# Kernel tuning notes

Hardware: AMD Instinct MI355X
Metric: run time of the kernel (lower is better)

## Reference

```python
import jax, jax.numpy as jnp
import numpy as np

EMA_DECAY = 0.99
LAPLACE_EPS = 1e-7
PERPLEXITY_EPS = 1e-10
COMMIT_COEF = 0.25


def setup_inputs() -> dict:
    key = jax.random.key(0)
    k1, k2, k3, k4 = jax.random.split(key, 4)
    B, C, T, H, W = 8, 256, 4, 32, 32
    n_codes = 2048
    z = jax.random.normal(k1, (B, C, T, H, W), dtype=jnp.float32)
    embeddings = jax.random.normal(k2, (n_codes, C), dtype=jnp.float32)
    N = jnp.ones((n_codes,), dtype=jnp.float32)  # state after _init_embeddings
    z_avg = jax.random.normal(k3, (n_codes, C), dtype=jnp.float32)
    k_rand = jax.random.normal(k4, (n_codes, C), dtype=jnp.float32)  # stand-in for randperm restart rows
    return {"z": z, "embeddings": embeddings, "N": N, "z_avg": z_avg, "k_rand": k_rand}


def reference(z, embeddings, N, z_avg, k_rand):
    b, c, t, h, w = z.shape
    n_codes = embeddings.shape[0]
    # rearrange 'b c t h w -> (b t h w) c'
    flat = jnp.transpose(z, (0, 2, 3, 4, 1)).reshape(-1, c)  # [Ntok, c]
    d2 = ((flat * flat).sum(axis=1, keepdims=True)
          - 2.0 * (flat @ embeddings.T)
          + (embeddings * embeddings).sum(axis=1)[None, :])  # [Ntok, n_codes]
    idx = jnp.argmin(d2, axis=1)  # [Ntok] int
    quant_flat = embeddings[idx]  # gather, [Ntok, c]
    # back to [b, c, t, h, w] (the double-rearrange in the torch code is a net permute back)
    quant = jnp.transpose(quant_flat.reshape(b, t, h, w, c), (0, 4, 1, 2, 3))
    commitment_loss = COMMIT_COEF * jnp.mean((z - jax.lax.stop_gradient(quant)) ** 2)
    embeddings_st = jax.lax.stop_gradient(quant - z) + z  # straight-through
    # EMA codebook update (one-hot scatter expressed as segment_sum)
    ones = jnp.ones(flat.shape[0], dtype=flat.dtype)
    counts = jax.ops.segment_sum(ones, idx, num_segments=n_codes)          # n_total
    encode_sum = jax.ops.segment_sum(flat, idx, num_segments=n_codes)      # [n_codes, c]
    new_N = N * EMA_DECAY + (1.0 - EMA_DECAY) * counts
    new_z_avg = z_avg * EMA_DECAY + (1.0 - EMA_DECAY) * encode_sum
    n = new_N.sum()
    weights = (new_N + LAPLACE_EPS) / (n + n_codes * LAPLACE_EPS) * n
    new_embeddings = new_z_avg / weights[:, None]
    usage = (new_N[:, None] >= 1.0).astype(flat.dtype)
    new_embeddings = new_embeddings * usage + k_rand * (1.0 - usage)
    # perplexity
    avg_probs = counts / flat.shape[0]
    perplexity = jnp.exp(-jnp.sum(avg_probs * jnp.log(avg_probs + PERPLEXITY_EPS)))
    encodings = idx.reshape(b, t, h, w)
    return embeddings_st, encodings, commitment_loss, perplexity, new_embeddings, new_N, new_z_avg
```

## Files before the change

### kernel.cpp

```cpp
#include <hip/hip_runtime.h>
#include <math.h>

#define NCODES 2048
#define CDIM   256
#define SPAT   4096
#define NTOK   32768
#define XSTR   260
#define EPI_TOK 32

#define ETILE    32
#define HALFCODE 1024
#define NTILES   (HALFCODE / ETILE)

typedef _Float16 half8  __attribute__((ext_vector_type(8)));
typedef float    f32x4  __attribute__((ext_vector_type(4)));

#define WS_ENORM  0
#define WS_COUNTS 2048
#define WS_LOSS   4096
#define WS_N      4097
#define WS_ESUM   4100
#define WS_IDX    528388
#define WS_OFF    561156
#define WS_CUR    563204
#define WS_SORT   565252
#define WS_SCODE  598020
#define WS_CAND   630788
#define WS_E16    761860
#define WS_XH     1024004

#define O_QUANT 0
#define O_ENC   8388608
#define O_LOSS  8421376
#define O_PERP  8421377
#define O_EMB   8421378
#define O_NN    8945666
#define O_ZAVG  8947714

__device__ inline void gl_lds16(const void* g, void* l) {
    __builtin_amdgcn_global_load_lds(
        (const __attribute__((address_space(1))) void*)g,
        (__attribute__((address_space(3))) void*)l, 16, 0, 0);
}

__device__ inline unsigned umn(unsigned a, unsigned b) { return a < b ? a : b; }
__device__ inline unsigned umx(unsigned a, unsigned b) { return a > b ? a : b; }
__device__ inline unsigned shflx16(unsigned v, int off) {
    return (unsigned)__shfl_xor((int)v, off, 16);
}

__global__ void k_ecvt(const float* __restrict__ emb, float* __restrict__ ws) {
    const int tid  = threadIdx.x;
    const int code = (blockIdx.x << 3) + (tid >> 5);
    const int cg   = tid & 31;
    const float* src = emb + (size_t)code * CDIM + (cg << 3);
    const float4 f0 = *(const float4*)src;
    const float4 f1 = *(const float4*)(src + 4);
    half8 h = { (_Float16)f0.x, (_Float16)f0.y, (_Float16)f0.z, (_Float16)f0.w,
                (_Float16)f1.x, (_Float16)f1.y, (_Float16)f1.z, (_Float16)f1.w };
    char* dst = (char*)(ws + WS_E16) + (size_t)code * 512 + ((cg ^ (code & 7)) << 4);
    *(half8*)dst = h;
    float s = f0.x * f0.x + f0.y * f0.y + f0.z * f0.z + f0.w * f0.w
            + f1.x * f1.x + f1.y * f1.y + f1.z * f1.z + f1.w * f1.w;
#pragma unroll
    for (int off = 16; off; off >>= 1) s += __shfl_down(s, off, 32);
    if (cg == 0) ws[WS_ENORM + code] = s;
}

__global__ __launch_bounds__(256, 3) void k_main(
    const float* __restrict__ z, float* __restrict__ ws)
{
    __shared__ half8 Es8[2][ETILE][32];

    const int tid = threadIdx.x;
    const int raw = blockIdx.x;
    const int xcd = raw & 7, sub = raw >> 3;
    const int tb  = xcd * 32 + (sub >> 1);
    const int ch  = sub & 1;
    const int b   = tb >> 5;
    const int s0  = (tb & 31) * 128;
    const float* zb = z + (size_t)b * CDIM * SPAT + s0;
    const char* e16g = (const char*)(ws + WS_E16) + (size_t)ch * HALFCODE * 512;

    const int l  = tid & 63, w = tid >> 6;
    const int lr = l & 15, lg = l >> 4;

    {
        char* dst = (char*)&Es8[0][0][0];
#pragma unroll
        for (int q = 0; q < 4; ++q) {
            const int off = ((q << 2) + w) << 10;
            gl_lds16(e16g + off + (l << 4), dst + off);
        }
    }

    half8 a[2][8];
#pragma unroll
    for (int as = 0; as < 2; ++as)
#pragma unroll
    for (int ks = 0; ks < 8; ++ks) {
        float v[8];
#pragma unroll
        for (int e = 0; e < 8; ++e)
            v[e] = zb[(size_t)(ks * 32 + lg * 8 + e) * SPAT + (w * 32 + as * 16 + lr)];
        half8 h = { (_Float16)v[0], (_Float16)v[1], (_Float16)v[2], (_Float16)v[3],
                    (_Float16)v[4], (_Float16)v[5], (_Float16)v[6], (_Float16)v[7] };
        a[as][ks] = h;
    }

    if (ch == 0) {
        _Float16* xh = (_Float16*)(ws + WS_XH);
#pragma unroll
        for (int as = 0; as < 2; ++as) {
            _Float16* xr = xh + (size_t)(b * SPAT + s0 + w * 32 + as * 16 + lr) * CDIM;
#pragma unroll
            for (int ks = 0; ks < 8; ++ks)
                *(half8*)(xr + ks * 32 + lg * 8) = a[as][ks];
        }
    }

    unsigned kb0[2][4], kb1[2][4];
#pragma unroll
    for (int as = 0; as < 2; ++as)
#pragma unroll
    for (int r = 0; r < 4; ++r) { kb0[as][r] = 0xFFFFFFFFu; kb1[as][r] = 0xFFFFFFFFu; }

    __syncthreads();

    int p = 0;
    for (int tile = 0; tile < NTILES; ++tile) {
        if (tile < NTILES - 1) {
            const char* src = e16g + (size_t)(tile + 1) * (ETILE * 512);
            char* dst = (char*)&Es8[p ^ 1][0][0];
#pragma unroll
            for (int q = 0; q < 4; ++q) {
                const int off = ((q << 2) + w) << 10;
                gl_lds16(src + off + (l << 4), dst + off);
            }
        }

        const float en0 = ws[WS_ENORM + ch * HALFCODE + tile * ETILE + lr];
        const float en1 = ws[WS_ENORM + ch * HALFCODE + tile * ETILE + 16 + lr];

        f32x4 acc[2][2];
#pragma unroll
        for (int as = 0; as < 2; ++as)
#pragma unroll
        for (int j = 0; j < 2; ++j) acc[as][j] = (f32x4)0.0f;

        half8 bf0[2], bf1[2];
#pragma unroll
        for (int j = 0; j < 2; ++j) {
            const int row = j * 16 + lr;
            bf0[j] = Es8[p][row][lg ^ (row & 7)];
        }
#pragma unroll
        for (int ks = 0; ks < 8; ++ks) {
            if (ks < 7) {
#pragma unroll
                for (int j = 0; j < 2; ++j) {
                    const int row = j * 16 + lr;
                    if (ks & 1) bf0[j] = Es8[p][row][((ks + 1) * 4 + lg) ^ (row & 7)];
                    else        bf1[j] = Es8[p][row][((ks + 1) * 4 + lg) ^ (row & 7)];
                }
            }
            __builtin_amdgcn_s_setprio(1);
#pragma unroll
            for (int as = 0; as < 2; ++as)
#pragma unroll
            for (int j = 0; j < 2; ++j)
                acc[as][j] = __builtin_amdgcn_mfma_f32_16x16x32_f16(
                    a[as][ks], (ks & 1) ? bf1[j] : bf0[j], acc[as][j], 0, 0, 0);
            __builtin_amdgcn_s_setprio(0);
        }

        const float enb0 = en0 + 4096.0f;
        const float enb1 = en1 + 4096.0f;
        const unsigned code0 = (unsigned)(ch * HALFCODE + tile * ETILE + lr);
        const unsigned code1 = code0 + 16u;
#pragma unroll
        for (int as = 0; as < 2; ++as)
#pragma unroll
        for (int r = 0; r < 4; ++r) {
            {
                const float d = fmaf(acc[as][0][r], -2.0f, enb0);
                const unsigned key = (__float_as_uint(d) & 0xFFFFF800u) | code0;
                const unsigned hi = umx(kb0[as][r], key);
                kb0[as][r] = umn(kb0[as][r], key);
                kb1[as][r] = umn(kb1[as][r], hi);
            }
            {
                const float d = fmaf(acc[as][1][r], -2.0f, enb1);
                const unsigned key = (__float_as_uint(d) & 0xFFFFF800u) | code1;
                const unsigned hi = umx(kb0[as][r], key);
                kb0[as][r] = umn(kb0[as][r], key);
                kb1[as][r] = umn(kb1[as][r], hi);
            }
        }

        __syncthreads();
        p ^= 1;
    }

#pragma unroll
    for (int as = 0; as < 2; ++as)
#pragma unroll
    for (int r = 0; r < 4; ++r) {
        unsigned k0 = kb0[as][r], k1 = kb1[as][r];
        unsigned k2 = 0xFFFFFFFFu, k3 = 0xFFFFFFFFu;
#pragma unroll
        for (int off = 8; off; off >>= 1) {
            const unsigned o0 = shflx16(k0, off);
            const unsigned o1 = shflx16(k1, off);
            const unsigned o2 = shflx16(k2, off);
            const unsigned o3 = shflx16(k3, off);
            const unsigned m0 = umn(k0, o3), m1 = umn(k1, o2);
            const unsigned m2 = umn(k2, o1), m3 = umn(k3, o0);
            const unsigned t0 = umn(m0, m2), t2 = umx(m0, m2);
            const unsigned t1 = umn(m1, m3), t3 = umx(m1, m3);
            k0 = umn(t0, t1); k1 = umx(t0, t1);
            k2 = umn(t2, t3); k3 = umx(t2, t3);
        }
        if (lr == 0) {
            const int tokg = b * SPAT + s0 + w * 32 + as * 16 + lg * 4 + r;
            ushort4 c4;
            c4.x = (unsigned short)(k0 & 2047u);
            c4.y = (unsigned short)(k1 & 2047u);
            c4.z = (unsigned short)(k2 & 2047u);
            c4.w = (unsigned short)(k3 & 2047u);
            *(ushort4*)((unsigned short*)((int*)ws + WS_CAND) + (size_t)tokg * 8 + ch * 4) = c4;
        }
    }
}

__global__ __launch_bounds__(256, 4) void k_epi(
    const float* __restrict__ z, const float* __restrict__ emb,
    float* __restrict__ ws, float* __restrict__ out)
{
    __shared__ float Xs[EPI_TOK * XSTR];
    __shared__ int   idxs[EPI_TOK];
    __shared__ float lloss[EPI_TOK];

    const int tid = threadIdx.x, blk = blockIdx.x;
    const int b   = blk >> 7;
    const int s0  = (blk & 127) * EPI_TOK;
    const float* zb = z + (size_t)b * CDIM * SPAT + s0;

    {
        const int s  = tid & 31;
        const int c0 = tid >> 5;
#pragma unroll 4
        for (int c = c0; c < CDIM; c += 8)
            Xs[s * XSTR + c] = zb[(size_t)c * SPAT + s];
    }
    __syncthreads();

    {
        const int t = tid >> 3, h = tid & 7;
        const unsigned short* cp =
            (const unsigned short*)((int*)ws + WS_CAND) + ((size_t)blk * EPI_TOK + t) * 8;
        const int mycand = cp[h];
        const float en_h = ws[WS_ENORM + mycand];

        int cand[8];
        {
            const ushort4 ca = *(const ushort4*)cp;
            const ushort4 cb = *(const ushort4*)(cp + 4);
            cand[0] = ca.x; cand[1] = ca.y; cand[2] = ca.z; cand[3] = ca.w;
            cand[4] = cb.x; cand[5] = cb.y; cand[6] = cb.z; cand[7] = cb.w;
        }

        float4 xq[8];
#pragma unroll
        for (int q = 0; q < 8; ++q)
            xq[q] = *(const float4*)&Xs[t * XSTR + q * 32 + h * 4];

        float xn = 0.0f;
#pragma unroll
        for (int q = 0; q < 8; ++q)
            xn += xq[q].x * xq[q].x + xq[q].y * xq[q].y
                + xq[q].z * xq[q].z + xq[q].w * xq[q].w;
        xn += __shfl_xor(xn, 1, 8);
        xn += __shfl_xor(xn, 2, 8);
        xn += __shfl_xor(xn, 4, 8);

        float p8[8];
#pragma unroll
        for (int k = 0; k < 8; ++k) {
            const float* er = emb + (size_t)cand[k] * CDIM + h * 4;
            float dp = 0.0f;
#pragma unroll
            for (int q = 0; q < 8; ++q) {
                const float4 e4 = *(const float4*)(er + q * 32);
                dp += xq[q].x * e4.x + xq[q].y * e4.y + xq[q].z * e4.z + xq[q].w * e4.w;
            }
            p8[k] = dp;
        }

        float np4[4];
#pragma unroll
        for (int k2 = 0; k2 < 4; ++k2) {
            const float own = (h & 1) ? p8[2 * k2 + 1] : p8[2 * k2];
            const float snd = (h & 1) ? p8[2 * k2]     : p8[2 * k2 + 1];
            np4[k2] = own + __shfl_xor(snd, 1, 8);
        }
        float nq2[2];
#pragma unroll
        for (int k3 = 0; k3 < 2; ++k3) {
            const float own = ((h >> 1) & 1) ? np4[2 * k3 + 1] : np4[2 * k3];
            const float snd = ((h >> 1) & 1) ? np4[2 * k3]     : np4[2 * k3 + 1];
            nq2[k3] = own + __shfl_xor(snd, 2, 8);
        }
        const float own = ((h >> 2) & 1) ? nq2[1] : nq2[0];
        const float snd = ((h >> 2) & 1) ? nq2[0] : nq2[1];
        const float dot = own + __shfl_xor(snd, 4, 8);

        float bd = en_h - 2.0f * dot;
        int   bi = mycand;
#pragma unroll
        for (int off = 4; off; off >>= 1) {
            const float od = __shfl_xor(bd, off, 8);
            const int   oi = __shfl_xor(bi, off, 8);
            if (od < bd || (od == bd && oi < bi)) { bd = od; bi = oi; }
        }
        if (h == 0) {
            idxs[t]  = bi;
            lloss[t] = xn + bd;
            out[O_ENC + blk * EPI_TOK + t] = (float)bi;
            ((int*)ws)[WS_IDX + blk * EPI_TOK + t] = bi;
            atomicAdd(ws + WS_COUNTS + bi, 1.0f);
        }
    }
    __syncthreads();

    {
        const int t = tid >> 3, h = tid & 7;
        const float* ewin = emb + (size_t)idxs[t] * CDIM + h * 4;
#pragma unroll
        for (int q = 0; q < 8; ++q)
            *(float4*)&Xs[t * XSTR + q * 32 + h * 4] = *(const float4*)(ewin + q * 32);
    }
    __syncthreads();

    {
        const int s  = tid & 31;
        const int c0 = tid >> 5;
        float* qcol = out + O_QUANT + (size_t)b * CDIM * SPAT + s0 + s;
#pragma unroll 4
        for (int c = c0; c < CDIM; c += 8)
            qcol[(size_t)c * SPAT] = Xs[s * XSTR + c];
    }
    if (tid == 0) {
        float ls = 0.0f;
#pragma unroll
        for (int t = 0; t < EPI_TOK; ++t) ls += lloss[t];
        atomicAdd(ws + WS_LOSS, ls);
    }
}

__global__ void k_finalize(const float* __restrict__ Nin, float* __restrict__ ws,
                           float* __restrict__ out) {
    __shared__ float r1[4], r2[4];
    __shared__ int   wsum[4];
    const int tid  = threadIdx.x;
    const int base = tid * 8;

    float cnt[8];
    {
        const float4 c0 = *(const float4*)(ws + WS_COUNTS + base);
        const float4 c1 = *(const float4*)(ws + WS_COUNTS + base + 4);
        cnt[0] = c0.x; cnt[1] = c0.y; cnt[2] = c0.z; cnt[3] = c0.w;
        cnt[4] = c1.x; cnt[5] = c1.y; cnt[6] = c1.z; cnt[7] = c1.w;
    }

    float nsum = 0.0f, H = 0.0f;
    int   tsum = 0;
#pragma unroll
    for (int j = 0; j < 8; ++j) {
        const float cf = cnt[j];
        const float nn = Nin[base + j] * 0.99f + 0.01f * cf;
        out[O_NN + base + j] = nn;
        nsum += nn;
        const float p = cf * (1.0f / 32768.0f);
        H += p * logf(p + 1e-10f);
        tsum += (int)cf;
    }

    int inc = tsum;
#pragma unroll
    for (int off = 1; off < 64; off <<= 1) {
        const int v = __shfl_up(inc, off, 64);
        if ((tid & 63) >= off) inc += v;
    }
    const int wv = tid >> 6, ln = tid & 63;
    if (ln == 63) wsum[wv] = inc;

#pragma unroll
    for (int off = 32; off; off >>= 1) {
        nsum += __shfl_down(nsum, off);
        H    += __shfl_down(H, off);
    }
    if (ln == 0) { r1[wv] = nsum; r2[wv] = H; }
    __syncthreads();

    int wbase = 0;
    for (int q = 0; q < wv; ++q) wbase += wsum[q];
    int run = wbase + inc - tsum;
    int* offp = (int*)ws + WS_OFF;
    int* curp = (int*)ws + WS_CUR;
#pragma unroll
    for (int j = 0; j < 8; ++j) {
        offp[base + j] = run;
        curp[base + j] = run;
        run += (int)cnt[j];
    }

    if (tid == 0) {
        const float nt = r1[0] + r1[1] + r1[2] + r1[3];
        const float Ht = r2[0] + r2[1] + r2[2] + r2[3];
        ws[WS_N] = nt;
        out[O_PERP] = expf(-Ht);
        out[O_LOSS] = 0.25f * ws[WS_LOSS] * (1.0f / 8388608.0f);
    }
}

__global__ void k_scatter(float* __restrict__ ws) {
    const int t    = blockIdx.x * 256 + threadIdx.x;
    const int code = ((const int*)ws)[WS_IDX + t];
    const int slot = atomicAdd((int*)ws + WS_CUR + code, 1);
    ((int*)ws)[WS_SORT  + slot] = t;
    ((int*)ws)[WS_SCODE + slot] = code;
}

__global__ __launch_bounds__(256) void k_gather(float* __restrict__ ws) {
    __shared__ int stok[64], scod[64];
    const int g = blockIdx.x, tid = threadIdx.x, c = tid;
    if (tid < 64) {
        stok[tid] = ((const int*)ws)[WS_SORT  + g * 64 + tid];
        scod[tid] = ((const int*)ws)[WS_SCODE + g * 64 + tid];
    }
    __syncthreads();

    const _Float16* xh = (const _Float16*)(ws + WS_XH);
    float* esum = ws + WS_ESUM;

    float acc = 0.0f;
    for (int k0 = 0; k0 < 64; k0 += 8) {
        float v[8];
#pragma unroll
        for (int j = 0; j < 8; ++j)
            v[j] = (float)xh[(size_t)stok[k0 + j] * CDIM + c];
#pragma unroll
        for (int j = 0; j < 8; ++j) {
            const int k = k0 + j;
            acc += v[j];
            if (k == 63 || scod[k] != scod[k + 1]) {
                atomicAdd(&esum[(size_t)scod[k] * CDIM + c], acc);
                acc = 0.0f;
            }
        }
    }
}

__global__ __launch_bounds__(256) void k_update(
    const float* __restrict__ zavg, const float* __restrict__ krand,
    const float* __restrict__ ws, float* __restrict__ out)
{
    const int i = blockIdx.x, c = threadIdx.x;
    const float nn  = out[O_NN + i];
    const float n   = ws[WS_N];
    const float wgt = (nn + 1e-7f) / (n + NCODES * 1e-7f) * n;
    const size_t o  = (size_t)i * CDIM + c;
    const float ez  = 0.99f * zavg[o] + 0.01f * ws[WS_ESUM + o];
    out[O_ZAVG + o] = ez;
    out[O_EMB + o]  = (nn >= 1.0f) ? (ez / wgt) : krand[o];
}

extern "C" void kernel_launch(void* const* d_in, const int* in_sizes, int n_in,
                              void* d_out, int out_size, void* d_ws, size_t ws_size,
                              hipStream_t stream) {
    const float* z     = (const float*)d_in[0];
    const float* emb   = (const float*)d_in[1];
    const float* Nin   = (const float*)d_in[2];
    const float* zavg  = (const float*)d_in[3];
    const float* krand = (const float*)d_in[4];
    float* out = (float*)d_out;
    float* ws  = (float*)d_ws;

    hipMemsetAsync(ws + WS_COUNTS, 0,
                   (size_t)(2048 + 4 + NCODES * CDIM) * sizeof(float), stream);

    k_ecvt    <<<NCODES / 8,  256, 0, stream>>>(emb, ws);
    k_main    <<<512,         256, 0, stream>>>(z, ws);
    k_epi     <<<1024,        256, 0, stream>>>(z, emb, ws, out);
    k_finalize<<<1,           256, 0, stream>>>(Nin, ws, out);
    k_scatter <<<NTOK / 256,  256, 0, stream>>>(ws);
    k_gather  <<<NTOK / 64,   256, 0, stream>>>(ws);
    k_update  <<<NCODES,      256, 0, stream>>>(zavg, krand, ws, out);
}
```

Measured before the change: 136.4 us.

## Triple-buffer codebook tiles in LDS with two-deep prefetch and partial waitcnt

Switches the codebook tile staging in the distance kernel from double to triple buffering, issuing async global-to-LDS loads two tiles ahead. Barriers wait only for the older batch of loads (vmcnt(4)) instead of draining all loads before every tile. The aim is to hide more global load latency behind the MFMA work. The cost is 50% more LDS per block, which may limit occupancy, and the hand-written vmcnt counts must stay correct, since the ws enorm loads also count as vector memory operations.

```diff
diff --git a/kernel.cpp b/kernel.cpp
--- a/kernel.cpp
+++ b/kernel.cpp
@@ -70,7 +70,7 @@
 __global__ __launch_bounds__(256, 3) void k_main(
     const float* __restrict__ z, float* __restrict__ ws)
 {
-    __shared__ half8 Es8[2][ETILE][32];
+    __shared__ half8 Es8[3][ETILE][32];
 
     const int tid = threadIdx.x;
     const int raw = blockIdx.x;
@@ -85,14 +85,16 @@
     const int l  = tid & 63, w = tid >> 6;
     const int lr = l & 15, lg = l >> 4;
 
-    {
-        char* dst = (char*)&Es8[0][0][0];
-#pragma unroll
-        for (int q = 0; q < 4; ++q) {
-            const int off = ((q << 2) + w) << 10;
-            gl_lds16(e16g + off + (l << 4), dst + off);
-        }
-    }
+#define STAGE(tileidx, bufidx) do {                                         \
+        const char* src_ = e16g + (size_t)(tileidx) * (ETILE * 512);        \
+        char* dst_ = (char*)&Es8[bufidx][0][0];                             \
+        _Pragma("unroll")                                                   \
+        for (int q_ = 0; q_ < 4; ++q_) {                                    \
+            const int off_ = ((q_ << 2) + w) << 10;                         \
+            gl_lds16(src_ + off_ + (l << 4), dst_ + off_);                  \
+        } } while (0)
+
+    STAGE(0, 0);
 
     half8 a[2][8];
 #pragma unroll
@@ -125,23 +127,13 @@
 #pragma unroll
     for (int r = 0; r < 4; ++r) { kb0[as][r] = 0xFFFFFFFFu; kb1[as][r] = 0xFFFFFFFFu; }
 
-    __syncthreads();
-
-    int p = 0;
-    for (int tile = 0; tile < NTILES; ++tile) {
-        if (tile < NTILES - 1) {
-            const char* src = e16g + (size_t)(tile + 1) * (ETILE * 512);
-            char* dst = (char*)&Es8[p ^ 1][0][0];
-#pragma unroll
-            for (int q = 0; q < 4; ++q) {
-                const int off = ((q << 2) + w) << 10;
-                gl_lds16(src + off + (l << 4), dst + off);
-            }
-        }
-
-        const float en0 = ws[WS_ENORM + ch * HALFCODE + tile * ETILE + lr];
-        const float en1 = ws[WS_ENORM + ch * HALFCODE + tile * ETILE + 16 + lr];
-
+    asm volatile("s_waitcnt vmcnt(0)" ::: "memory");
+    __builtin_amdgcn_s_barrier();
+    __builtin_amdgcn_sched_barrier(0);
+
+    STAGE(1, 1);
+
+    auto compute_tile = [&](int bp, int tile, float en0, float en1) {
         f32x4 acc[2][2];
 #pragma unroll
         for (int as = 0; as < 2; ++as)
@@ -152,7 +144,7 @@
 #pragma unroll
         for (int j = 0; j < 2; ++j) {
             const int row = j * 16 + lr;
-            bf0[j] = Es8[p][row][lg ^ (row & 7)];
+            bf0[j] = Es8[bp][row][lg ^ (row & 7)];
         }
 #pragma unroll
         for (int ks = 0; ks < 8; ++ks) {
@@ -160,8 +152,8 @@
 #pragma unroll
                 for (int j = 0; j < 2; ++j) {
                     const int row = j * 16 + lr;
-                    if (ks & 1) bf0[j] = Es8[p][row][((ks + 1) * 4 + lg) ^ (row & 7)];
-                    else        bf1[j] = Es8[p][row][((ks + 1) * 4 + lg) ^ (row & 7)];
+                    if (ks & 1) bf0[j] = Es8[bp][row][((ks + 1) * 4 + lg) ^ (row & 7)];
+                    else        bf1[j] = Es8[bp][row][((ks + 1) * 4 + lg) ^ (row & 7)];
                 }
             }
             __builtin_amdgcn_s_setprio(1);
@@ -197,10 +189,32 @@
                 kb1[as][r] = umn(kb1[as][r], hi);
             }
         }
-
-        __syncthreads();
-        p ^= 1;
-    }
+    };
+
+    int p = 0;
+    for (int tile = 0; tile < NTILES; ++tile) {
+        const float en0 = ws[WS_ENORM + ch * HALFCODE + tile * ETILE + lr];
+        const float en1 = ws[WS_ENORM + ch * HALFCODE + tile * ETILE + 16 + lr];
+
+        if (tile + 2 < NTILES) {
+            const int p2 = (p + 2 >= 3) ? p - 1 : p + 2;
+            STAGE(tile + 2, p2);
+        }
+
+        compute_tile(p, tile, en0, en1);
+
+        if (tile + 2 < NTILES) {
+            asm volatile("s_waitcnt vmcnt(4)" ::: "memory");
+            __builtin_amdgcn_s_barrier();
+            __builtin_amdgcn_sched_barrier(0);
+        } else if (tile + 2 == NTILES) {
+            asm volatile("s_waitcnt vmcnt(0)" ::: "memory");
+            __builtin_amdgcn_s_barrier();
+            __builtin_amdgcn_sched_barrier(0);
+        }
+        p = (p == 2) ? 0 : p + 1;
+    }
+#undef STAGE
 
 #pragma unroll
     for (int as = 0; as < 2; ++as)
```

Result: slower. 140.2 us (+2.8%).
